# Performance work log

Hardware: AMD Instinct MI355X
Metric: run time of the kernel (lower is better)

## Reference

```python
import math
import jax, jax.numpy as jnp
import numpy as np

N_EXPERTS = 8
CAPACITY_FACTOR = 1.25
AUX_COEF = 0.01  # forward passes aux_loss_coef to BOTH z-loss and lb-loss


def setup_inputs() -> dict:
    key = jax.random.key(0)
    k1, k2 = jax.random.split(key)
    B, T, D = 4, 4096, 2048
    x = jax.random.normal(k1, (B, T, D), dtype=jnp.float32)
    # nn.Linear(d_model, n_experts, bias=False) weight: (n_experts, d_model)
    W = jax.random.normal(k2, (N_EXPERTS, D), dtype=jnp.float32) * (1.0 / math.sqrt(D))
    return {"x": x, "W": W}


def reference(x, W):
    B, T, D = x.shape
    S = B * T
    E = W.shape[0]
    capacity = int(math.ceil(S / E * CAPACITY_FACTOR))  # static

    x_flat = x.reshape(S, D)
    logits = jnp.einsum("sd,ed->se", x_flat, W)          # (S, E)
    probs = jax.nn.softmax(logits, axis=-1)               # (S, E)
    gate_vals = jnp.max(probs, axis=-1)                   # (S,)
    expert_idx = jnp.argmax(probs, axis=-1)               # (S,) int

    # rank of each token within its expert's queue (token order), 0-based
    onehot = jax.nn.one_hot(expert_idx, E, dtype=jnp.int32)        # (S, E)
    rank = jnp.sum(jnp.cumsum(onehot, axis=0) * onehot, axis=-1) - 1  # (S,)
    keep = rank < capacity
    kept_gates = jnp.where(keep, gate_vals, jnp.zeros((), gate_vals.dtype))

    # z-loss: coef * mean(logsumexp(logits)^2)
    log_z = jax.scipy.special.logsumexp(logits, axis=-1)
    z_loss = AUX_COEF * jnp.mean(log_z * log_z)

    # load-balance loss: coef * E * sum(f_i * p_i)
    p = jnp.mean(probs, axis=0)                                     # (E,)
    counts = jnp.zeros((E,), dtype=probs.dtype).at[expert_idx].add(1.0)
    f = counts / S
    lb_loss = AUX_COEF * E * jnp.sum(f * p)

    aux_loss = z_loss + lb_loss
    return expert_idx, kept_gates, aux_loss
```

## Files before the change

### kernel.cpp

```cpp
#include <hip/hip_runtime.h>

#define S_TOKENS 16384
#define DMODEL   2048
#define NE       8
#define CAPACITY 2560


__global__ __launch_bounds__(512) void logits_kernel(
    const float* __restrict__ x, const float* __restrict__ W,
    int* __restrict__ idx_out, float* __restrict__ gate_out,
    float* __restrict__ partials) {
    __shared__ float4 Ws4[NE][DMODEL/4];
    __shared__ float  sacc[16];

    const int tid  = threadIdx.x;
    const int wave = tid >> 6;
    const int lane = tid & 63;

    if (tid < 16) sacc[tid] = 0.0f;
    {
        const float4* __restrict__ Wg = (const float4*)W;
        float4* Wl = (float4*)Ws4;
        #pragma unroll
        for (int i = 0; i < 8; ++i) Wl[i*512 + tid] = Wg[i*512 + tid];
    }
    __syncthreads();

    const int token0 = blockIdx.x * 32 + wave * 4;
    const float4* __restrict__ x0 = (const float4*)(x + (size_t)token0 * DMODEL);
    const float4* __restrict__ x1 = x0 + 512;
    const float4* __restrict__ x2 = x0 + 1024;
    const float4* __restrict__ x3 = x0 + 1536;

    float a0[NE], a1[NE], a2[NE], a3[NE];
    #pragma unroll
    for (int e = 0; e < NE; ++e) { a0[e]=0; a1[e]=0; a2[e]=0; a3[e]=0; }

    #pragma unroll 2
    for (int i = 0; i < 8; ++i) {
        const int j4 = i*64 + lane;
        float4 xv0 = x0[j4];
        float4 xv1 = x1[j4];
        float4 xv2 = x2[j4];
        float4 xv3 = x3[j4];
        #pragma unroll
        for (int e = 0; e < NE; ++e) {
            float4 w = Ws4[e][j4];
            a0[e] += xv0.x*w.x + xv0.y*w.y + xv0.z*w.z + xv0.w*w.w;
            a1[e] += xv1.x*w.x + xv1.y*w.y + xv1.z*w.z + xv1.w*w.w;
            a2[e] += xv2.x*w.x + xv2.y*w.y + xv2.z*w.z + xv2.w*w.w;
            a3[e] += xv3.x*w.x + xv3.y*w.y + xv3.z*w.z + xv3.w*w.w;
        }
    }

    const bool hiHalf = (lane & 32) != 0;
    const bool oddQ   = (lane & 16) != 0;
    float lg[NE];
    #pragma unroll
    for (int e = 0; e < NE; ++e) {
        float s0 = a0[e] + __shfl_xor(a0[e], 32);
        float s1 = a1[e] + __shfl_xor(a1[e], 32);
        float s2 = a2[e] + __shfl_xor(a2[e], 32);
        float s3 = a3[e] + __shfl_xor(a3[e], 32);
        float u = hiHalf ? s2 : s0;
        float v = hiHalf ? s3 : s1;
        u += __shfl_xor(u, 16);
        v += __shfl_xor(v, 16);
        float r = oddQ ? v : u;
        r += __shfl_xor(r, 8);
        r += __shfl_xor(r, 4);
        r += __shfl_xor(r, 2);
        r += __shfl_xor(r, 1);
        lg[e] = r;
    }

    const int token = token0 + (lane >> 4);
    const int sub   = lane & 15;

    float m = lg[0]; int e = 0;
    #pragma unroll
    for (int k = 1; k < NE; ++k) { if (lg[k] > m) { m = lg[k]; e = k; } }
    float z = 0.0f;
    #pragma unroll
    for (int k = 0; k < NE; ++k) z += expf(lg[k] - m);
    float gate = 1.0f / z;
    float lz   = m + logf(z);

    if (sub == 0) {
        idx_out[token]  = e;
        gate_out[token] = gate;
        atomicAdd(&sacc[8], lz * lz);
    }
    if (sub < NE) {
        float b0 = (sub & 1) ? lg[1] : lg[0];
        float b1 = (sub & 1) ? lg[3] : lg[2];
        float b2 = (sub & 1) ? lg[5] : lg[4];
        float b3 = (sub & 1) ? lg[7] : lg[6];
        float c0 = (sub & 2) ? b1 : b0;
        float c1 = (sub & 2) ? b3 : b2;
        float ae = (sub & 4) ? c1 : c0;
        atomicAdd(&sacc[sub], expf(ae - m) * gate);
    }

    __syncthreads();
    if (tid < 9) partials[tid*512 + blockIdx.x] = sacc[tid];
}

__global__ __launch_bounds__(1024) void scan_kernel(
    const int* __restrict__ idx, const float* __restrict__ partials,
    int* __restrict__ prefix, float* __restrict__ aux_out) {
    __shared__ float facc[9];
    __shared__ int   cnt[256][9];
    const int t    = threadIdx.x;
    const int wv   = t >> 6;
    const int lane = t & 63;

    if (t < 9) facc[t] = 0.0f;
    __syncthreads();

    if (t < 512) {
        #pragma unroll
        for (int q = 0; q < 9; ++q) {
            float v = partials[q*512 + t];
            #pragma unroll
            for (int off = 32; off > 0; off >>= 1) v += __shfl_xor(v, off);
            if (lane == 0) atomicAdd(&facc[q], v);
        }
    }

    {
        const int s0 = wv * 16;
        int ev[16];
        #pragma unroll
        for (int k = 0; k < 16; ++k) ev[k] = idx[(s0+k)*64 + lane];
        #pragma unroll
        for (int k = 0; k < 16; ++k) {
            #pragma unroll
            for (int q = 0; q < NE; ++q) {
                unsigned long long mk = __ballot(ev[k] == q);
                if (lane == q) cnt[s0+k][q] = (int)__popcll(mk);
            }
        }
    }
    __syncthreads();

    int myc[NE];
    if (t < 256) {
        #pragma unroll
        for (int q = 0; q < NE; ++q) myc[q] = cnt[t][q];
    }
    for (int off = 1; off < 256; off <<= 1) {
        int v[NE];
        if (t < 256) {
            #pragma unroll
            for (int q = 0; q < NE; ++q) v[q] = (t >= off) ? cnt[t-off][q] : 0;
        }
        __syncthreads();
        if (t < 256) {
            #pragma unroll
            for (int q = 0; q < NE; ++q) cnt[t][q] += v[q];
        }
        __syncthreads();
    }

    if (t < 256) {
        #pragma unroll
        for (int q = 0; q < NE; ++q) prefix[t*8 + q] = cnt[t][q] - myc[q];
    }
    if (t == 0) {
        float lb = 0.0f;
        #pragma unroll
        for (int q = 0; q < NE; ++q) {
            float f = (float)cnt[255][q] * (1.0f/S_TOKENS);
            float p = facc[q] * (1.0f/S_TOKENS);
            lb += f * p;
        }
        aux_out[0] = 0.01f * (facc[8] * (1.0f/S_TOKENS)) + 0.08f * lb;
    }
}

__global__ __launch_bounds__(64) void output_kernel(
    const int* __restrict__ idx, const float* __restrict__ gate,
    const int* __restrict__ prefix, float* __restrict__ out) {
    const int b = blockIdx.x;
    const int l = threadIdx.x;
    const int token = b*64 + l;
    const int e = idx[token];
    const float g = gate[token];

    unsigned long long mymask = 0;
    #pragma unroll
    for (int q = 0; q < NE; ++q) {
        unsigned long long mk = __ballot(e == q);
        if (e == q) mymask = mk;
    }
    unsigned long long lt = (1ull << l) - 1ull;
    int rank = prefix[b*8 + e] + (int)__popcll(mymask & lt);

    out[token] = (float)e;
    out[S_TOKENS + token] = (rank < CAPACITY) ? g : 0.0f;
}

extern "C" void kernel_launch(void* const* d_in, const int* in_sizes, int n_in,
                              void* d_out, int out_size, void* d_ws, size_t ws_size,
                              hipStream_t stream) {
    const float* x = (const float*)d_in[0];
    const float* W = (const float*)d_in[1];
    float* out = (float*)d_out;

    int*   ws_idx    = (int*)d_ws;
    float* ws_gate   = (float*)d_ws + 16384;
    float* ws_part   = (float*)d_ws + 32768;
    int*   ws_prefix = (int*)d_ws + 37376;

    logits_kernel<<<512, 512, 0, stream>>>(x, W, ws_idx, ws_gate, ws_part);
    scan_kernel<<<1, 1024, 0, stream>>>(ws_idx, ws_part, ws_prefix, out + 2*S_TOKENS);
    output_kernel<<<256, 64, 0, stream>>>(ws_idx, ws_gate, ws_prefix, out);
}
```

Measured before the change: 211.0 us.

## Compute per-block expert histograms in logits kernel and fuse scan into output kernel

The logits kernel now also writes a per-block (32-token) expert histogram to workspace. The single-block scan kernel and the output kernel are replaced by one tail kernel. In it, each 64-token block sums the histograms of all earlier blocks to get its prefix, and one extra block reduces the aux-loss partials. This removes a serial single-workgroup scan and one kernel launch, at the cost of redundant prefix summation that grows with block index.

New measurement: 220.6 us. 1.05x slower.

```diff
diff --git a/kernel.cpp b/kernel.cpp
--- a/kernel.cpp
+++ b/kernel.cpp
@@ -9,15 +9,17 @@
 __global__ __launch_bounds__(512) void logits_kernel(
     const float* __restrict__ x, const float* __restrict__ W,
     int* __restrict__ idx_out, float* __restrict__ gate_out,
-    float* __restrict__ partials) {
+    float* __restrict__ partials, int* __restrict__ hist) {
     __shared__ float4 Ws4[NE][DMODEL/4];
     __shared__ float  sacc[16];
+    __shared__ int    shist[8];
 
     const int tid  = threadIdx.x;
     const int wave = tid >> 6;
     const int lane = tid & 63;
 
     if (tid < 16) sacc[tid] = 0.0f;
+    if (tid < 8)  shist[tid] = 0;
     {
         const float4* __restrict__ Wg = (const float4*)W;
         float4* Wl = (float4*)Ws4;
@@ -90,6 +92,7 @@
         idx_out[token]  = e;
         gate_out[token] = gate;
         atomicAdd(&sacc[8], lz * lz);
+        atomicAdd(&shist[e], 1);
     }
     if (sub < NE) {
         float b0 = (sub & 1) ? lg[1] : lg[0];
@@ -104,101 +107,67 @@
 
     __syncthreads();
     if (tid < 9) partials[tid*512 + blockIdx.x] = sacc[tid];
+    if (tid < 8) hist[blockIdx.x*8 + tid] = shist[tid];
 }
 
-__global__ __launch_bounds__(1024) void scan_kernel(
-    const int* __restrict__ idx, const float* __restrict__ partials,
-    int* __restrict__ prefix, float* __restrict__ aux_out) {
-    __shared__ float facc[9];
-    __shared__ int   cnt[256][9];
-    const int t    = threadIdx.x;
-    const int wv   = t >> 6;
-    const int lane = t & 63;
+__global__ __launch_bounds__(64) void tail_kernel(
+    const int* __restrict__ idx, const float* __restrict__ gate,
+    const float* __restrict__ partials, const int* __restrict__ hist,
+    float* __restrict__ out) {
+    const int b = blockIdx.x;
+    const int l = threadIdx.x;
 
-    if (t < 9) facc[t] = 0.0f;
-    __syncthreads();
+    if (b < 256) {
+        const int token = b*64 + l;
+        const int e = idx[token];
+        const float g = gate[token];
 
-    if (t < 512) {
+        int acc = 0;
+        const int jend = 2*b;
+        for (int j = (l >> 3); j < jend; j += 8) acc += hist[j*8 + (l & 7)];
+        acc += __shfl_xor(acc, 8);
+        acc += __shfl_xor(acc, 16);
+        acc += __shfl_xor(acc, 32);
+        const int myprefix = __shfl(acc, e);
+
+        unsigned long long mymask = 0;
+        #pragma unroll
+        for (int q = 0; q < NE; ++q) {
+            unsigned long long mk = __ballot(e == q);
+            if (e == q) mymask = mk;
+        }
+        const unsigned long long lt = (1ull << l) - 1ull;
+        const int rank = myprefix + (int)__popcll(mymask & lt);
+
+        out[token] = (float)e;
+        out[S_TOKENS + token] = (rank < CAPACITY) ? g : 0.0f;
+    } else {
+        float vq[9];
         #pragma unroll
         for (int q = 0; q < 9; ++q) {
-            float v = partials[q*512 + t];
+            float v = 0.0f;
+            for (int j = l; j < 512; j += 64) v += partials[q*512 + j];
             #pragma unroll
             for (int off = 32; off > 0; off >>= 1) v += __shfl_xor(v, off);
-            if (lane == 0) atomicAdd(&facc[q], v);
+            vq[q] = v;
         }
-    }
+        int acc = 0;
+        for (int j = (l >> 3); j < 512; j += 8) acc += hist[j*8 + (l & 7)];
+        acc += __shfl_xor(acc, 8);
+        acc += __shfl_xor(acc, 16);
+        acc += __shfl_xor(acc, 32);
 
-    {
-        const int s0 = wv * 16;
-        int ev[16];
-        #pragma unroll
-        for (int k = 0; k < 16; ++k) ev[k] = idx[(s0+k)*64 + lane];
-        #pragma unroll
-        for (int k = 0; k < 16; ++k) {
-            #pragma unroll
-            for (int q = 0; q < NE; ++q) {
-                unsigned long long mk = __ballot(ev[k] == q);
-                if (lane == q) cnt[s0+k][q] = (int)__popcll(mk);
-            }
-        }
-    }
-    __syncthreads();
-
-    int myc[NE];
-    if (t < 256) {
-        #pragma unroll
-        for (int q = 0; q < NE; ++q) myc[q] = cnt[t][q];
-    }
-    for (int off = 1; off < 256; off <<= 1) {
-        int v[NE];
-        if (t < 256) {
-            #pragma unroll
-            for (int q = 0; q < NE; ++q) v[q] = (t >= off) ? cnt[t-off][q] : 0;
-        }
-        __syncthreads();
-        if (t < 256) {
-            #pragma unroll
-            for (int q = 0; q < NE; ++q) cnt[t][q] += v[q];
-        }
-        __syncthreads();
-    }
-
-    if (t < 256) {
-        #pragma unroll
-        for (int q = 0; q < NE; ++q) prefix[t*8 + q] = cnt[t][q] - myc[q];
-    }
-    if (t == 0) {
         float lb = 0.0f;
         #pragma unroll
         for (int q = 0; q < NE; ++q) {
-            float f = (float)cnt[255][q] * (1.0f/S_TOKENS);
-            float p = facc[q] * (1.0f/S_TOKENS);
-            lb += f * p;
+            float cq = (float)__shfl(acc, q);
+            lb += cq * vq[q];
         }
-        aux_out[0] = 0.01f * (facc[8] * (1.0f/S_TOKENS)) + 0.08f * lb;
+        if (l == 0) {
+            const float invS = 1.0f / S_TOKENS;
+            out[2*S_TOKENS] = 0.01f * (vq[8] * invS) + 0.08f * (lb * invS * invS);
+        }
     }
-}
-
-__global__ __launch_bounds__(64) void output_kernel(
-    const int* __restrict__ idx, const float* __restrict__ gate,
-    const int* __restrict__ prefix, float* __restrict__ out) {
-    const int b = blockIdx.x;
-    const int l = threadIdx.x;
-    const int token = b*64 + l;
-    const int e = idx[token];
-    const float g = gate[token];
-
-    unsigned long long mymask = 0;
-    #pragma unroll
-    for (int q = 0; q < NE; ++q) {
-        unsigned long long mk = __ballot(e == q);
-        if (e == q) mymask = mk;
-    }
-    unsigned long long lt = (1ull << l) - 1ull;
-    int rank = prefix[b*8 + e] + (int)__popcll(mymask & lt);
-
-    out[token] = (float)e;
-    out[S_TOKENS + token] = (rank < CAPACITY) ? g : 0.0f;
 }
 
 extern "C" void kernel_launch(void* const* d_in, const int* in_sizes, int n_in,
@@ -208,12 +177,11 @@
     const float* W = (const float*)d_in[1];
     float* out = (float*)d_out;
 
-    int*   ws_idx    = (int*)d_ws;
-    float* ws_gate   = (float*)d_ws + 16384;
-    float* ws_part   = (float*)d_ws + 32768;
-    int*   ws_prefix = (int*)d_ws + 37376;
+    int*   ws_idx  = (int*)d_ws;
+    float* ws_gate = (float*)d_ws + 16384;
+    float* ws_part = (float*)d_ws + 32768;
+    int*   ws_hist = (int*)d_ws + 37376;
 
-    logits_kernel<<<512, 512, 0, stream>>>(x, W, ws_idx, ws_gate, ws_part);
-    scan_kernel<<<1, 1024, 0, stream>>>(ws_idx, ws_part, ws_prefix, out + 2*S_TOKENS);
-    output_kernel<<<256, 64, 0, stream>>>(ws_idx, ws_gate, ws_prefix, out);
+    logits_kernel<<<512, 512, 0, stream>>>(x, W, ws_idx, ws_gate, ws_part, ws_hist);
+    tail_kernel<<<257, 64, 0, stream>>>(ws_idx, ws_gate, ws_part, ws_hist, out);
 }
```
